# Performance work log

Measured on AMD Instinct MI355X. Metric: run time of the kernel, lower is better.

## Reference

```python
import jax, jax.numpy as jnp
import numpy as np

ENC_DIM = 512
B, T = 2048, 256
NUM_PARTS, PART_DIM, ATT_DIM, VOCAB = 64, 32, 128, 12


def _p(key, shape, scale=0.05):
    return jax.random.normal(key, shape, dtype=jnp.float32) * scale


def setup_inputs() -> dict:
    key = jax.random.key(0)
    ks = jax.random.split(key, 24)
    inp = {
        "img_features": jax.random.normal(ks[0], (B, 32, 8, 8), dtype=jnp.float32),
        "label": jax.random.normal(ks[1], (B, T, VOCAB), dtype=jnp.float32),
        # Attention params
        "Ww": _p(ks[2], (ATT_DIM, PART_DIM)), "Wb": _p(ks[3], (ATT_DIM,)),
        "Uw": _p(ks[4], (ATT_DIM, ENC_DIM)), "Ub": _p(ks[5], (ATT_DIM,)),
        "vw": _p(ks[6], (1, ATT_DIM)), "vb": _p(ks[7], (1,)),
        "betaw": _p(ks[8], (PART_DIM, ENC_DIM)), "betab": _p(ks[9], (PART_DIM,)),
        # init hidden params
        "ihw": _p(ks[10], (ENC_DIM, NUM_PARTS)), "ihb": _p(ks[11], (ENC_DIM,)),
        "icw": _p(ks[12], (ENC_DIM, NUM_PARTS)), "icb": _p(ks[13], (ENC_DIM,)),
        # LSTMCell params (PyTorch layout: [4*H, in] / [4*H, H])
        "W_ih": _p(ks[14], (4 * ENC_DIM, VOCAB + PART_DIM)),
        "W_hh": _p(ks[15], (4 * ENC_DIM, ENC_DIM)),
        "b_ih": _p(ks[16], (4 * ENC_DIM,)), "b_hh": _p(ks[17], (4 * ENC_DIM,)),
        # output fc
        "ow": _p(ks[18], (VOCAB, ENC_DIM)), "ob": _p(ks[19], (VOCAB,)),
    }
    return inp


def reference(img_features, label, Ww, Wb, Uw, Ub, vw, vb, betaw, betab,
              ihw, ihb, icw, icb, W_ih, W_hh, b_ih, b_hh, ow, ob):
    b = img_features.shape[0]
    feats = img_features.reshape(b, 32, -1)          # [B, 32, 64]
    parts = feats.transpose(0, 2, 1)                  # [B, 64, 32]
    # init hidden/cell from mean over channel dim (dim=1 in torch)
    avg = feats.mean(axis=1)                          # [B, 64]
    h0 = jnp.tanh(avg @ ihw.T + ihb)                  # [B, H]
    c0 = jnp.tanh(avg @ icw.T + icb)
    # W_s depends only on img features: hoist out of the loop (same math)
    Ws = parts @ Ww.T + Wb                            # [B, 64, 128]
    lab = label.transpose(1, 0, 2)                    # [T, B, 12]

    H = h0.shape[1]

    def step(carry, x_t):
        h, c = carry
        Uh = h @ Uw.T + Ub                            # [B, 128]
        att = jnp.tanh(Ws + Uh[:, None, :])           # [B, 64, 128]
        score = (att @ vw.T + vb)[..., 0]             # [B, 64]
        alpha = jax.nn.softmax(score, axis=1)
        ctx = jnp.einsum('bp,bpd->bd', alpha, parts)  # [B, 32]
        beta = jax.nn.sigmoid(h @ betaw.T + betab)
        ctx = ctx * beta
        inp = jnp.concatenate([x_t, ctx], axis=1)     # [B, 44]
        gates = inp @ W_ih.T + b_ih + h @ W_hh.T + b_hh
        i, f, g, o = jnp.split(gates, 4, axis=1)
        c2 = jax.nn.sigmoid(f) * c + jax.nn.sigmoid(i) * jnp.tanh(g)
        h2 = jax.nn.sigmoid(o) * jnp.tanh(c2)
        out = h2 @ ow.T + ob                          # [B, 12]
        return (h2, c2), (out, alpha)

    (_, _), (outs, alphas) = jax.lax.scan(step, (h0, c0), lab)
    output = jax.nn.log_softmax(outs, axis=-1).transpose(1, 0, 2)  # [B, T, 12]
    return output, alphas  # alphas: [T, B, 64] (stacked version of the list)
```

## Files before the change

### kernel.cpp

```cpp
#include <hip/hip_runtime.h>
#include <hip/hip_bf16.h>


typedef __attribute__((ext_vector_type(8))) short short8;
typedef __attribute__((ext_vector_type(4))) float floatx4;
typedef __attribute__((ext_vector_type(2))) unsigned int uint2v;

#define DEV static __device__ __forceinline__
#define C2LE 2.885390082f
#define LOG2E 1.4426950409f
#define LN2 0.6931471806f

DEV unsigned short f2bf(float f) {
    unsigned int u = __float_as_uint(f);
    unsigned int r = (u + 0x7FFFu + ((u >> 16) & 1u)) >> 16;
    return (unsigned short)r;
}
DEV float bf2f(unsigned short u) { return __uint_as_float(((unsigned int)u) << 16); }
DEV float rcp_f(float x) { float r; asm("v_rcp_f32 %0, %1" : "=v"(r) : "v"(x)); return r; }
DEV float tanh_f(float x) { return 1.f - 2.f * rcp_f(1.f + exp2f(x * C2LE)); }
DEV float sigm(float x) { return rcp_f(1.f + exp2f(-x * LOG2E)); }

DEV void ldg16_sc(short8* d, const unsigned short* p) {
    asm volatile("global_load_dwordx4 %0, %1, off sc0 sc1" : "=v"(*d) : "v"(p));
}
DEV void stg16_sc(unsigned short* p, short8 v) {
    asm volatile("global_store_dwordx4 %0, %1, off sc0 sc1" :: "v"(p), "v"(v) : "memory");
}
DEV void stg8_sc(unsigned short* p, uint2v v) {
    asm volatile("global_store_dwordx2 %0, %1, off sc0 sc1" :: "v"(p), "v"(v) : "memory");
}
DEV void st_flag(int* p, int v) {
    asm volatile("global_store_dword %0, %1, off sc0 sc1" :: "v"(p), "v"(v) : "memory");
}
DEV int ld_flag(const int* p) {
    int v;
    asm volatile("global_load_dword %0, %1, off sc0 sc1\n\ts_waitcnt vmcnt(0)"
                 : "=v"(v) : "v"(p) : "memory");
    return v;
}
DEV void waitv0() { asm volatile("s_waitcnt vmcnt(0)" ::: "memory"); }

#define OFF_XH     ((size_t)0)
#define OFF_C0     ((size_t)2359296)
#define OFF_PARTS  ((size_t)6553600)
#define OFF_WBIG   ((size_t)14942208)
#define OFF_WSMALL ((size_t)17301504)
#define OFF_WW2    ((size_t)17465344)
#define OFF_BIAS   ((size_t)17473536)
#define OFF_AVG    ((size_t)17481728)
#define OFF_FLAGS  ((size_t)18006016)

DEV void gbar(int* flags, int bk, int g4, int step) {
    waitv0();
    __syncthreads();
    if (threadIdx.x < 64) {
        int lane = threadIdx.x;
        if (lane == 0) st_flag(flags + bk * 32, step);
        for (;;) {
            int v = step;
            if (lane < 4) v = ld_flag(flags + (g4 + lane) * 32);
            if (__all(v >= step)) break;
            __builtin_amdgcn_s_sleep(1);
        }
    }
    __syncthreads();
}

__global__ void k_init(int* flags) {
    int i = blockIdx.x * 256 + threadIdx.x;
    if (i < 512 * 32) flags[i] = 0;
}

__global__ void k_avg(const float* __restrict__ img, float* __restrict__ avg) {
    int idx = blockIdx.x * 256 + threadIdx.x;
    int b = idx >> 6, p = idx & 63;
    const float* base = img + (size_t)b * 2048 + p;
    float s = 0.f;
#pragma unroll
    for (int k = 0; k < 32; ++k) s += base[k * 64];
    avg[idx] = s * (1.f / 32.f);
}

__global__ void k_prep(const float* __restrict__ Whh, const float* __restrict__ Wih,
                       const float* __restrict__ Uw, const float* __restrict__ betaw,
                       const float* __restrict__ Ww, const float* __restrict__ bih,
                       const float* __restrict__ bhh,
                       unsigned short* __restrict__ Wbig, unsigned short* __restrict__ Wsmall,
                       unsigned short* __restrict__ Ww2, float* __restrict__ bias_cat) {
    int p = blockIdx.x, tid = threadIdx.x;
    int g = p & 3, j = p >> 2, orig = g * 512 + j;
    for (int k = tid; k < 576; k += 256) {
        float v = 0.f;
        if (k < 512) v = Whh[(size_t)orig * 512 + k];
        else if (k < 556) v = Wih[(size_t)orig * 44 + (k - 512)];
        Wbig[(size_t)p * 576 + k] = f2bf(v);
    }
    if (p < 160) {
        for (int k = tid; k < 512; k += 256) {
            float v = (p < 128) ? Uw[(size_t)p * 512 + k] : betaw[(size_t)(p - 128) * 512 + k];
            Wsmall[(size_t)p * 512 + k] = f2bf(v);
        }
    }
    if (p < 128 && tid < 32) Ww2[p * 32 + tid] = f2bf(C2LE * Ww[p * 32 + tid]);
    if (tid == 0) bias_cat[orig] = bih[orig] + bhh[orig];
}

__global__ __launch_bounds__(512) void k_h0c0(const float* __restrict__ avg,
                                              const float* __restrict__ ihw, const float* __restrict__ ihb,
                                              const float* __restrict__ icw, const float* __restrict__ icb,
                                              unsigned short* __restrict__ xh, float* __restrict__ c0) {
    __shared__ float avg_s[8][64];
    int b0 = blockIdx.x * 8, tid = threadIdx.x;
    for (int i = tid; i < 8 * 64; i += 512) avg_s[i >> 6][i & 63] = avg[b0 * 64 + i];
    __syncthreads();
    int j = tid;
    float w0[64];
#pragma unroll
    for (int p4 = 0; p4 < 16; ++p4) {
        float4 v = ((const float4*)(ihw + j * 64))[p4];
        w0[p4 * 4 + 0] = v.x; w0[p4 * 4 + 1] = v.y; w0[p4 * 4 + 2] = v.z; w0[p4 * 4 + 3] = v.w;
    }
    float bh = ihb[j];
#pragma unroll
    for (int bb = 0; bb < 8; ++bb) {
        float s = bh;
#pragma unroll
        for (int p = 0; p < 64; ++p) s += w0[p] * avg_s[bb][p];
        xh[(size_t)(b0 + bb) * 576 + j] = f2bf(tanh_f(s));
        if (j < 20) xh[(size_t)(b0 + bb) * 576 + 556 + j] = 0;
    }
#pragma unroll
    for (int p4 = 0; p4 < 16; ++p4) {
        float4 v = ((const float4*)(icw + j * 64))[p4];
        w0[p4 * 4 + 0] = v.x; w0[p4 * 4 + 1] = v.y; w0[p4 * 4 + 2] = v.z; w0[p4 * 4 + 3] = v.w;
    }
    float bc = icb[j];
#pragma unroll
    for (int bb = 0; bb < 8; ++bb) {
        float s = bc;
#pragma unroll
        for (int p = 0; p < 64; ++p) s += w0[p] * avg_s[bb][p];
        c0[(size_t)(b0 + bb) * 512 + j] = tanh_f(s);
    }
}

__global__ __launch_bounds__(256) void k_parts(const float* __restrict__ img,
                                               unsigned short* __restrict__ parts_bf) {
    __shared__ float pl[64][33];
    int b = blockIdx.x, tid = threadIdx.x;
    const float* ib = img + (size_t)b * 2048;
    for (int i = tid; i < 2048; i += 256) pl[i & 63][i >> 6] = ib[i];
    __syncthreads();
    for (int i = tid; i < 2048; i += 256)
        parts_bf[(size_t)b * 2048 + i] = f2bf(pl[i >> 5][i & 31]);
}

__global__ __launch_bounds__(256, 2) void k_scan(
    unsigned short* __restrict__ xh,
    const float* __restrict__ c0,
    const unsigned short* __restrict__ parts_bf,
    const unsigned short* __restrict__ Wsmall, const unsigned short* __restrict__ Wbig,
    const unsigned short* __restrict__ Ww2, const float* __restrict__ bias_cat,
    const float* __restrict__ Ub, const float* __restrict__ betab, const float* __restrict__ Wb,
    const float* __restrict__ vw,
    const float* __restrict__ label, const float* __restrict__ ow, const float* __restrict__ ob,
    float* __restrict__ out_alpha, float* __restrict__ out_logits,
    int* __restrict__ flags)
{
    __shared__ unsigned short Ald[16 * 584];
    __shared__ unsigned short ow_l[12][512];
    __shared__ unsigned short h2scr[16][128];
    __shared__ float uh_l[16][160];
    __shared__ float al_l[4][64];
    __shared__ float bias_l[512];
    __shared__ unsigned short xscr[4][48];
    __shared__ float vw2_l[128];
    __shared__ float obl[12];

    const int tid = threadIdx.x, w = tid >> 6, lane = tid & 63;
    const int bk = blockIdx.x;
    const int mtile = bk >> 2, ntile = bk & 3;
    const int g4 = bk & ~3;

    if (tid < 128) vw2_l[tid] = -2.f * vw[tid];
    if (tid < 12) obl[tid] = ob[tid];
    for (int i = tid; i < 512; i += 256) {
        int g = i >> 7, jl = i & 127;
        bias_l[i] = bias_cat[g * 512 + ntile * 128 + jl];
    }
    for (int i = tid; i < 12 * 512; i += 256) ow_l[i >> 9][i & 511] = f2bf(ow[i]);
    for (int i = tid; i < 16 * 20; i += 256) {
        int row = i / 20, cc = 556 + (i % 20);
        Ald[row * 584 + cc] = 0;
    }
    float creg[32];
#pragma unroll
    for (int nf = 0; nf < 8; ++nf)
#pragma unroll
        for (int r = 0; r < 4; ++r) {
            int b = mtile * 16 + (lane >> 4) * 4 + r;
            int j = ntile * 128 + w * 32 + nf * 4 + (lane & 3);
            creg[nf * 4 + r] = c0[(size_t)b * 512 + j];
        }

    floatx4 acc[8];
    float vwsum = 0.f;

    auto stage16 = [&]() {
        short8 tv[4];
#pragma unroll
        for (int q = 0; q < 4; ++q) {
            int cid = tid + q * 256;
            int row = cid >> 6, c16 = cid & 63;
            ldg16_sc(&tv[q], xh + (size_t)(mtile * 16 + row) * 576 + c16 * 8);
        }
        waitv0();
        __builtin_amdgcn_sched_barrier(0);
#pragma unroll
        for (int q = 0; q < 4; ++q) {
            int cid = tid + q * 256;
            int row = cid >> 6, c16 = cid & 63;
            *(short8*)&Ald[row * 584 + c16 * 8] = tv[q];
        }
    };
    auto stage_tail = [&]() {
        if (tid < 128) {
            short8 tv;
            int row = tid >> 3, c16 = tid & 7;
            ldg16_sc(&tv, xh + (size_t)(mtile * 16 + row) * 576 + 512 + c16 * 8);
            waitv0();
            __builtin_amdgcn_sched_barrier(0);
            *(short8*)&Ald[row * 584 + 512 + c16 * 8] = tv;
        }
    };

    auto do_uh = [&]() {
        for (int nt = w; nt < 10; nt += 4) {
            const unsigned short* Bp = Wsmall + (size_t)(nt * 16 + (lane & 15)) * 512 + (lane >> 4) * 8;
            const unsigned short* Ab = &Ald[(lane & 15) * 584 + (lane >> 4) * 8];
            floatx4 u = {};
#pragma unroll 4
            for (int k0 = 0; k0 < 512; k0 += 32) {
                short8 a = *(const short8*)(Ab + k0);
                u = __builtin_amdgcn_mfma_f32_16x16x32_bf16(a, *(const short8*)(Bp + k0), u, 0, 0, 0);
            }
            int n = nt * 16 + (lane & 15), r0 = (lane >> 4) * 4;
            float addv = (n < 128) ? (Ub[n] + Wb[n]) : betab[n - 128];
            float scl = (n < 128) ? C2LE : 1.f;
#pragma unroll
            for (int r = 0; r < 4; ++r) uh_l[r0 + r][n] = (u[r] + addv) * scl;
        }
    };

    auto do_head = [&](int tt) {
        int lr = ntile * 4 + w;
        int b = bk * 4 + w;
        short8 hv = *(const short8*)&Ald[lr * 584 + lane * 8];
        float hf[8];
#pragma unroll
        for (int j = 0; j < 8; ++j) hf[j] = bf2f((unsigned short)hv[j]);
        float ov[12];
#pragma unroll
        for (int v = 0; v < 12; ++v) {
            short8 wv = *(const short8*)&ow_l[v][lane * 8];
            float p = 0.f;
#pragma unroll
            for (int j = 0; j < 8; ++j) p += hf[j] * bf2f((unsigned short)wv[j]);
#pragma unroll
            for (int o = 32; o; o >>= 1) p += __shfl_xor(p, o);
            ov[v] = p + obl[v];
        }
        float mx = ov[0];
#pragma unroll
        for (int v = 1; v < 12; ++v) mx = fmaxf(mx, ov[v]);
        float ss = 0.f;
#pragma unroll
        for (int v = 0; v < 12; ++v) ss += exp2f((ov[v] - mx) * LOG2E);
        float lse = mx + log2f(ss) * LN2;
#pragma unroll
        for (int v = 0; v < 12; ++v)
            if (lane == v) out_logits[((size_t)b * 256 + tt) * 12 + v] = ov[v] - lse;
    };

    auto do_attn = [&](int tt) {
        int lr = ntile * 4 + w;
        int b = bk * 4 + w;
        const unsigned short* pb = parts_bf + (size_t)b * 2048;
        short8 pa[4];
#pragma unroll
        for (int mt = 0; mt < 4; ++mt)
            pa[mt] = *(const short8*)(pb + ((lane & 15) + 16 * mt) * 32 + (lane >> 4) * 8);
        float sc[4][4] = {};
#pragma unroll
        for (int nt = 0; nt < 8; ++nt) {
            short8 wwf = *(const short8*)(Ww2 + (size_t)((lane & 15) + 16 * nt) * 32 + (lane >> 4) * 8);
            int d = nt * 16 + (lane & 15);
            float ud = uh_l[lr][d];
            float v2 = vw2_l[d];
            floatx4 ini = {ud, ud, ud, ud};
#pragma unroll
            for (int mt = 0; mt < 4; ++mt) {
                floatx4 wsa = __builtin_amdgcn_mfma_f32_16x16x32_bf16(pa[mt], wwf, ini, 0, 0, 0);
#pragma unroll
                for (int r = 0; r < 4; ++r)
                    sc[mt][r] += v2 * rcp_f(1.f + exp2f(wsa[r]));
            }
        }
        float mx = -1e30f;
#pragma unroll
        for (int mt = 0; mt < 4; ++mt)
#pragma unroll
            for (int r = 0; r < 4; ++r) {
                float s = sc[mt][r];
                s += __shfl_xor(s, 1); s += __shfl_xor(s, 2);
                s += __shfl_xor(s, 4); s += __shfl_xor(s, 8);
                s += vwsum;
                sc[mt][r] = s;
                mx = fmaxf(mx, s);
            }
        mx = fmaxf(mx, __shfl_xor(mx, 16));
        mx = fmaxf(mx, __shfl_xor(mx, 32));
        float ssum = 0.f;
        float av[4][4];
#pragma unroll
        for (int mt = 0; mt < 4; ++mt)
#pragma unroll
            for (int r = 0; r < 4; ++r) {
                av[mt][r] = exp2f((sc[mt][r] - mx) * LOG2E);
                ssum += av[mt][r];
            }
        ssum += __shfl_xor(ssum, 16);
        ssum += __shfl_xor(ssum, 32);
        float rs = rcp_f(ssum);
#pragma unroll
        for (int mt = 0; mt < 4; ++mt) {
            if ((lane & 15) == mt) {
                float4 fv = make_float4(av[mt][0] * rs, av[mt][1] * rs, av[mt][2] * rs, av[mt][3] * rs);
                int p0 = mt * 16 + (lane >> 4) * 4;
                *(float4*)&out_alpha[((size_t)tt * 2048 + b) * 64 + p0] = fv;
                *(float4*)&al_l[w][p0] = fv;
            }
        }
        int k = lane & 31, half = lane >> 5;
        float cp = 0.f;
#pragma unroll
        for (int p = 0; p < 32; ++p) {
            int pp = half * 32 + p;
            cp += al_l[w][pp] * bf2f(pb[pp * 32 + k]);
        }
        cp += __shfl_xor(cp, 32);
        if (half == 0) xscr[w][12 + k] = f2bf(cp * sigm(uh_l[lr][128 + k]));
        if (lane < 12) xscr[w][lane] = f2bf(label[((size_t)b * 256 + tt) * 12 + lane]);
        if (lane < 11) {
            uint2v v = *(const uint2v*)&xscr[w][lane * 4];
            stg8_sc(xh + (size_t)b * 576 + 512 + lane * 4, v);
        }
    };

    auto gemm_h = [&]() {
        const unsigned short* Bp = Wbig + (size_t)(ntile * 512 + w * 128 + (lane & 15)) * 576 + (lane >> 4) * 8;
        const unsigned short* Ab = &Ald[(lane & 15) * 584 + (lane >> 4) * 8];
#pragma unroll
        for (int nf = 0; nf < 8; ++nf) acc[nf] = (floatx4){0.f, 0.f, 0.f, 0.f};
#pragma unroll 2
        for (int kk = 0; kk < 16; ++kk) {
            int k0 = kk * 32;
            short8 a = *(const short8*)(Ab + k0);
#pragma unroll
            for (int nf = 0; nf < 8; ++nf) {
                short8 bv = *(const short8*)(Bp + (size_t)nf * 9216 + k0);
                acc[nf] = __builtin_amdgcn_mfma_f32_16x16x32_bf16(a, bv, acc[nf], 0, 0, 0);
            }
        }
    };
    auto gemm_tail_cell = [&]() {
        const unsigned short* Bp = Wbig + (size_t)(ntile * 512 + w * 128 + (lane & 15)) * 576 + (lane >> 4) * 8;
        const unsigned short* Ab = &Ald[(lane & 15) * 584 + (lane >> 4) * 8];
#pragma unroll
        for (int kk = 16; kk < 18; ++kk) {
            int k0 = kk * 32;
            short8 a = *(const short8*)(Ab + k0);
#pragma unroll
            for (int nf = 0; nf < 8; ++nf) {
                short8 bv = *(const short8*)(Bp + (size_t)nf * 9216 + k0);
                acc[nf] = __builtin_amdgcn_mfma_f32_16x16x32_bf16(a, bv, acc[nf], 0, 0, 0);
            }
        }
        int base = (lane & 48) | ((lane & 3) * 4);
#pragma unroll
        for (int nf = 0; nf < 8; ++nf) {
            int jl = w * 32 + nf * 4 + (lane & 3);
            float bi = bias_l[jl], bfv = bias_l[128 + jl], bg = bias_l[256 + jl], bo = bias_l[384 + jl];
#pragma unroll
            for (int r = 0; r < 4; ++r) {
                float x = acc[nf][r];
                float g0 = __shfl(x, base + 0);
                float g1 = __shfl(x, base + 1);
                float g2 = __shfl(x, base + 2);
                float g3 = __shfl(x, base + 3);
                int ci = nf * 4 + r;
                float c2 = sigm(g1 + bfv) * creg[ci] + sigm(g0 + bi) * tanh_f(g2 + bg);
                creg[ci] = c2;
                float h2 = sigm(g3 + bo) * tanh_f(c2);
                if (((lane >> 2) & 3) == 0) {
                    int row = (lane >> 4) * 4 + r;
                    h2scr[row][jl] = f2bf(h2);
                }
            }
        }
        __syncthreads();
        {
            int row = tid >> 4, seg = tid & 15;
            short8 v = *(const short8*)&h2scr[row][seg * 8];
            stg16_sc(xh + (size_t)(mtile * 16 + row) * 576 + ntile * 128 + seg * 8, v);
        }
    };

    stage16();
    __syncthreads();
    {
        float s = 0.f;
#pragma unroll
        for (int d = 0; d < 128; ++d) s += vw2_l[d];
        vwsum = -0.5f * s;
    }
    do_uh();
    __syncthreads();
    do_attn(0);

    int bc = 0;
    for (int t = 0; t < 256; ++t) {
        gemm_h();
        gbar(flags, bk, g4, ++bc);
        stage_tail();
        __syncthreads();
        gemm_tail_cell();
        gbar(flags, bk, g4, ++bc);
        stage16();
        __syncthreads();
        do_head(t);
        if (t < 255) {
            do_uh();
            __syncthreads();
            do_attn(t + 1);
        }
    }
}

extern "C" void kernel_launch(void* const* d_in, const int* in_sizes, int n_in,
                              void* d_out, int out_size, void* d_ws, size_t ws_size,
                              hipStream_t stream) {
    const float* img   = (const float*)d_in[0];
    const float* label = (const float*)d_in[1];
    const float* Ww    = (const float*)d_in[2];
    const float* Wb    = (const float*)d_in[3];
    const float* Uw    = (const float*)d_in[4];
    const float* Ub    = (const float*)d_in[5];
    const float* vw    = (const float*)d_in[6];
    const float* betaw = (const float*)d_in[8];
    const float* betab = (const float*)d_in[9];
    const float* ihw   = (const float*)d_in[10];
    const float* ihb   = (const float*)d_in[11];
    const float* icw   = (const float*)d_in[12];
    const float* icb   = (const float*)d_in[13];
    const float* Wih   = (const float*)d_in[14];
    const float* Whh   = (const float*)d_in[15];
    const float* bih   = (const float*)d_in[16];
    const float* bhh   = (const float*)d_in[17];
    const float* ow    = (const float*)d_in[18];
    const float* ob    = (const float*)d_in[19];

    char* ws = (char*)d_ws;
    unsigned short* xh       = (unsigned short*)(ws + OFF_XH);
    float*          c0       = (float*)(ws + OFF_C0);
    unsigned short* parts_bf = (unsigned short*)(ws + OFF_PARTS);
    unsigned short* Wbig     = (unsigned short*)(ws + OFF_WBIG);
    unsigned short* Wsmall   = (unsigned short*)(ws + OFF_WSMALL);
    unsigned short* Ww2      = (unsigned short*)(ws + OFF_WW2);
    float*          bias     = (float*)(ws + OFF_BIAS);
    float*          avg      = (float*)(ws + OFF_AVG);
    int*            flags    = (int*)(ws + OFF_FLAGS);

    float* out_logits = (float*)d_out;
    float* out_alpha  = out_logits + (size_t)2048 * 256 * 12;

    k_init<<<64, 256, 0, stream>>>(flags);
    k_avg<<<512, 256, 0, stream>>>(img, avg);
    k_prep<<<2048, 256, 0, stream>>>(Whh, Wih, Uw, betaw, Ww, bih, bhh, Wbig, Wsmall, Ww2, bias);
    k_h0c0<<<256, 512, 0, stream>>>(avg, ihw, ihb, icw, icb, xh, c0);
    k_parts<<<2048, 256, 0, stream>>>(img, parts_bf);

    k_scan<<<512, 256, 0, stream>>>(xh, c0, parts_bf, Wsmall, Wbig, Ww2, bias,
                                    Ub, betab, Wb, vw, label, ow, ob,
                                    out_alpha, out_logits, flags);
}
```

Measured before the change: 14.30 ms.

## Interleave two batch halves per block to hide group-barrier waits

The persistent scan kernel now runs on 256 blocks, each handling two independent 16-row batch chunks (A and B) with double-buffered LDS and separate cell-state registers. The combined barrier is split into post and wait, so one chunk's gate GEMM or attention runs while the other chunk's flag barrier is still pending. The gate GEMM is also merged into a single 18-step K loop instead of a split h/tail pass around a barrier. This halves the grid and doubles register and LDS use per block, which may lower occupancy, in exchange for hiding cross-block synchronization latency.

```diff
diff --git a/kernel.cpp b/kernel.cpp
--- a/kernel.cpp
+++ b/kernel.cpp
@@ -51,25 +51,9 @@
 #define OFF_AVG    ((size_t)17481728)
 #define OFF_FLAGS  ((size_t)18006016)
 
-DEV void gbar(int* flags, int bk, int g4, int step) {
-    waitv0();
-    __syncthreads();
-    if (threadIdx.x < 64) {
-        int lane = threadIdx.x;
-        if (lane == 0) st_flag(flags + bk * 32, step);
-        for (;;) {
-            int v = step;
-            if (lane < 4) v = ld_flag(flags + (g4 + lane) * 32);
-            if (__all(v >= step)) break;
-            __builtin_amdgcn_s_sleep(1);
-        }
-    }
-    __syncthreads();
-}
-
 __global__ void k_init(int* flags) {
     int i = blockIdx.x * 256 + threadIdx.x;
-    if (i < 512 * 32) flags[i] = 0;
+    if (i < 256 * 32) flags[i] = 0;
 }
 
 __global__ void k_avg(const float* __restrict__ img, float* __restrict__ avg) {
@@ -168,7 +152,7 @@
     float* __restrict__ out_alpha, float* __restrict__ out_logits,
     int* __restrict__ flags)
 {
-    __shared__ unsigned short Ald[16 * 584];
+    __shared__ unsigned short Ald[2][16 * 584];
     __shared__ unsigned short ow_l[12][512];
     __shared__ unsigned short h2scr[16][128];
     __shared__ float uh_l[16][160];
@@ -190,30 +174,52 @@
         bias_l[i] = bias_cat[g * 512 + ntile * 128 + jl];
     }
     for (int i = tid; i < 12 * 512; i += 256) ow_l[i >> 9][i & 511] = f2bf(ow[i]);
-    for (int i = tid; i < 16 * 20; i += 256) {
-        int row = i / 20, cc = 556 + (i % 20);
-        Ald[row * 584 + cc] = 0;
-    }
-    float creg[32];
+#pragma unroll
+    for (int c = 0; c < 2; ++c)
+        for (int i = tid; i < 16 * 20; i += 256) {
+            int row = i / 20, cc = 556 + (i % 20);
+            Ald[c][row * 584 + cc] = 0;
+        }
+    float cregA[32], cregB[32];
 #pragma unroll
     for (int nf = 0; nf < 8; ++nf)
 #pragma unroll
         for (int r = 0; r < 4; ++r) {
-            int b = mtile * 16 + (lane >> 4) * 4 + r;
+            int br = mtile * 16 + (lane >> 4) * 4 + r;
             int j = ntile * 128 + w * 32 + nf * 4 + (lane & 3);
-            creg[nf * 4 + r] = c0[(size_t)b * 512 + j];
-        }
-
-    floatx4 acc[8];
+            cregA[nf * 4 + r] = c0[(size_t)br * 512 + j];
+            cregB[nf * 4 + r] = c0[(size_t)(1024 + br) * 512 + j];
+        }
+
     float vwsum = 0.f;
-
-    auto stage16 = [&]() {
+    int bc = 0;
+    int xpostA = 0, xpostB = 0, hpostA = 0, hpostB = 0;
+
+    auto post = [&]() {
+        waitv0();
+        __syncthreads();
+        if (tid == 0) st_flag(flags + bk * 32, bc + 1);
+        ++bc;
+    };
+    auto wait_n = [&](int n) {
+        if (tid < 64) {
+            for (;;) {
+                int v = n;
+                if (lane < 4) v = ld_flag(flags + (g4 + lane) * 32);
+                if (__all(v >= n)) break;
+                __builtin_amdgcn_s_sleep(1);
+            }
+        }
+        __syncthreads();
+    };
+
+    auto stage16 = [&](unsigned short* A, int cb) {
         short8 tv[4];
 #pragma unroll
         for (int q = 0; q < 4; ++q) {
             int cid = tid + q * 256;
             int row = cid >> 6, c16 = cid & 63;
-            ldg16_sc(&tv[q], xh + (size_t)(mtile * 16 + row) * 576 + c16 * 8);
+            ldg16_sc(&tv[q], xh + (size_t)(cb + row) * 576 + c16 * 8);
         }
         waitv0();
         __builtin_amdgcn_sched_barrier(0);
@@ -221,24 +227,23 @@
         for (int q = 0; q < 4; ++q) {
             int cid = tid + q * 256;
             int row = cid >> 6, c16 = cid & 63;
-            *(short8*)&Ald[row * 584 + c16 * 8] = tv[q];
-        }
-    };
-    auto stage_tail = [&]() {
+            *(short8*)&A[row * 584 + c16 * 8] = tv[q];
+        }
+    };
+    auto stage_tail = [&](unsigned short* A, int cb) {
         if (tid < 128) {
             short8 tv;
             int row = tid >> 3, c16 = tid & 7;
-            ldg16_sc(&tv, xh + (size_t)(mtile * 16 + row) * 576 + 512 + c16 * 8);
+            ldg16_sc(&tv, xh + (size_t)(cb + row) * 576 + 512 + c16 * 8);
             waitv0();
             __builtin_amdgcn_sched_barrier(0);
-            *(short8*)&Ald[row * 584 + 512 + c16 * 8] = tv;
-        }
-    };
-
-    auto do_uh = [&]() {
+            *(short8*)&A[row * 584 + 512 + c16 * 8] = tv;
+        }
+    };
+    auto do_uh = [&](const unsigned short* A) {
         for (int nt = w; nt < 10; nt += 4) {
             const unsigned short* Bp = Wsmall + (size_t)(nt * 16 + (lane & 15)) * 512 + (lane >> 4) * 8;
-            const unsigned short* Ab = &Ald[(lane & 15) * 584 + (lane >> 4) * 8];
+            const unsigned short* Ab = &A[(lane & 15) * 584 + (lane >> 4) * 8];
             floatx4 u = {};
 #pragma unroll 4
             for (int k0 = 0; k0 < 512; k0 += 32) {
@@ -252,11 +257,10 @@
             for (int r = 0; r < 4; ++r) uh_l[r0 + r][n] = (u[r] + addv) * scl;
         }
     };
-
-    auto do_head = [&](int tt) {
+    auto do_head = [&](const unsigned short* A, int cb, int tt) {
         int lr = ntile * 4 + w;
-        int b = bk * 4 + w;
-        short8 hv = *(const short8*)&Ald[lr * 584 + lane * 8];
+        int b = cb + lr;
+        short8 hv = *(const short8*)&A[lr * 584 + lane * 8];
         float hf[8];
 #pragma unroll
         for (int j = 0; j < 8; ++j) hf[j] = bf2f((unsigned short)hv[j]);
@@ -282,10 +286,9 @@
         for (int v = 0; v < 12; ++v)
             if (lane == v) out_logits[((size_t)b * 256 + tt) * 12 + v] = ov[v] - lse;
     };
-
-    auto do_attn = [&](int tt) {
+    auto do_attn = [&](int cb, int tt) {
         int lr = ntile * 4 + w;
-        int b = bk * 4 + w;
+        int b = cb + lr;
         const unsigned short* pb = parts_bf + (size_t)b * 2048;
         short8 pa[4];
 #pragma unroll
@@ -357,28 +360,14 @@
             stg8_sc(xh + (size_t)b * 576 + 512 + lane * 4, v);
         }
     };
-
-    auto gemm_h = [&]() {
+    auto gemm_cell = [&](const unsigned short* A, int cb, float* creg) {
         const unsigned short* Bp = Wbig + (size_t)(ntile * 512 + w * 128 + (lane & 15)) * 576 + (lane >> 4) * 8;
-        const unsigned short* Ab = &Ald[(lane & 15) * 584 + (lane >> 4) * 8];
+        const unsigned short* Ab = &A[(lane & 15) * 584 + (lane >> 4) * 8];
+        floatx4 acc[8];
 #pragma unroll
         for (int nf = 0; nf < 8; ++nf) acc[nf] = (floatx4){0.f, 0.f, 0.f, 0.f};
 #pragma unroll 2
-        for (int kk = 0; kk < 16; ++kk) {
-            int k0 = kk * 32;
-            short8 a = *(const short8*)(Ab + k0);
-#pragma unroll
-            for (int nf = 0; nf < 8; ++nf) {
-                short8 bv = *(const short8*)(Bp + (size_t)nf * 9216 + k0);
-                acc[nf] = __builtin_amdgcn_mfma_f32_16x16x32_bf16(a, bv, acc[nf], 0, 0, 0);
-            }
-        }
-    };
-    auto gemm_tail_cell = [&]() {
-        const unsigned short* Bp = Wbig + (size_t)(ntile * 512 + w * 128 + (lane & 15)) * 576 + (lane >> 4) * 8;
-        const unsigned short* Ab = &Ald[(lane & 15) * 584 + (lane >> 4) * 8];
-#pragma unroll
-        for (int kk = 16; kk < 18; ++kk) {
+        for (int kk = 0; kk < 18; ++kk) {
             int k0 = kk * 32;
             short8 a = *(const short8*)(Ab + k0);
 #pragma unroll
@@ -413,11 +402,14 @@
         {
             int row = tid >> 4, seg = tid & 15;
             short8 v = *(const short8*)&h2scr[row][seg * 8];
-            stg16_sc(xh + (size_t)(mtile * 16 + row) * 576 + ntile * 128 + seg * 8, v);
-        }
-    };
-
-    stage16();
+            stg16_sc(xh + (size_t)(cb + row) * 576 + ntile * 128 + seg * 8, v);
+        }
+    };
+
+    const int cbA = mtile * 16, cbB = 1024 + mtile * 16;
+
+    stage16(Ald[0], cbA);
+    stage16(Ald[1], cbB);
     __syncthreads();
     {
         float s = 0.f;
@@ -425,25 +417,45 @@
         for (int d = 0; d < 128; ++d) s += vw2_l[d];
         vwsum = -0.5f * s;
     }
-    do_uh();
+    do_uh(Ald[0]);
     __syncthreads();
-    do_attn(0);
-
-    int bc = 0;
+    do_attn(cbA, 0);
+    post(); xpostA = bc;
+    do_uh(Ald[1]);
+    __syncthreads();
+    do_attn(cbB, 0);
+    post(); xpostB = bc;
+
     for (int t = 0; t < 256; ++t) {
-        gemm_h();
-        gbar(flags, bk, g4, ++bc);
-        stage_tail();
-        __syncthreads();
-        gemm_tail_cell();
-        gbar(flags, bk, g4, ++bc);
-        stage16();
-        __syncthreads();
-        do_head(t);
+        wait_n(xpostA);
+        stage_tail(Ald[0], cbA);
+        __syncthreads();
+        gemm_cell(Ald[0], cbA, cregA);
+        post(); hpostA = bc;
+        wait_n(xpostB);
+        stage_tail(Ald[1], cbB);
+        __syncthreads();
+        gemm_cell(Ald[1], cbB, cregB);
+        post(); hpostB = bc;
+        wait_n(hpostA);
+        stage16(Ald[0], cbA);
+        __syncthreads();
+        do_head(Ald[0], cbA, t);
         if (t < 255) {
-            do_uh();
+            do_uh(Ald[0]);
             __syncthreads();
-            do_attn(t + 1);
+            do_attn(cbA, t + 1);
+            post(); xpostA = bc;
+        }
+        wait_n(hpostB);
+        stage16(Ald[1], cbB);
+        __syncthreads();
+        do_head(Ald[1], cbB, t);
+        if (t < 255) {
+            do_uh(Ald[1]);
+            __syncthreads();
+            do_attn(cbB, t + 1);
+            post(); xpostB = bc;
         }
     }
 }
@@ -485,13 +497,13 @@
     float* out_logits = (float*)d_out;
     float* out_alpha  = out_logits + (size_t)2048 * 256 * 12;
 
-    k_init<<<64, 256, 0, stream>>>(flags);
+    k_init<<<32, 256, 0, stream>>>(flags);
     k_avg<<<512, 256, 0, stream>>>(img, avg);
     k_prep<<<2048, 256, 0, stream>>>(Whh, Wih, Uw, betaw, Ww, bih, bhh, Wbig, Wsmall, Ww2, bias);
     k_h0c0<<<256, 512, 0, stream>>>(avg, ihw, ihb, icw, icb, xh, c0);
     k_parts<<<2048, 256, 0, stream>>>(img, parts_bf);
 
-    k_scan<<<512, 256, 0, stream>>>(xh, c0, parts_bf, Wsmall, Wbig, Ww2, bias,
+    k_scan<<<256, 256, 0, stream>>>(xh, c0, parts_bf, Wsmall, Wbig, Ww2, bias,
                                     Ub, betab, Wb, vw, label, ow, ob,
                                     out_alpha, out_logits, flags);
 }
```

Measured after the change: 33.03 ms. 131% more time.
